# Optimization experiments

Measured on AMD Instinct MI355X. Metric: run time of the kernel, lower is better.

Reference implementation:

```python
import jax, jax.numpy as jnp
from jax import lax
import numpy as np

B, N, FIN, T, K, C_CHEB, F_TIME, STRIDE = 32, 900, 16, 24, 3, 64, 64, 1
LN_EPS = 1e-5


def _cheb_polys(L_tilde, K):
    # Faithful to repo: recurrence uses ELEMENTWISE multiply (np.ndarray '*').
    polys = [np.identity(N), np.asarray(L_tilde)]
    for i in range(2, K):
        polys.append(2 * L_tilde * polys[i - 1] - polys[i - 2])
    return np.stack(polys, axis=0).astype(np.float32)  # (K, N, N)


def setup_inputs() -> dict:
    key = jax.random.key(0)
    ks = jax.random.split(key, 6)
    rng = np.random.RandomState(0)
    A = rng.randn(N, N).astype(np.float32)
    L_tilde = (A + A.T) / (2.0 * np.sqrt(N))  # symmetric, entries O(1/sqrt(N))
    cheb = jnp.asarray(_cheb_polys(L_tilde, K))  # (K, N, N)
    x = jax.random.normal(ks[0], (B, N, FIN, T), dtype=jnp.float32)
    theta = jax.random.normal(ks[1], (K, FIN, C_CHEB), dtype=jnp.float32) * 0.1
    time_w = jax.random.normal(ks[2], (F_TIME, C_CHEB, 1, 3), dtype=jnp.float32) * 0.05
    time_b = jax.random.normal(ks[3], (F_TIME,), dtype=jnp.float32) * 0.01
    res_w = jax.random.normal(ks[4], (F_TIME, FIN, 1, 1), dtype=jnp.float32) * 0.1
    res_b = jax.random.normal(ks[5], (F_TIME,), dtype=jnp.float32) * 0.01
    gamma = jnp.ones((F_TIME,), dtype=jnp.float32)
    beta = jnp.zeros((F_TIME,), dtype=jnp.float32)
    return {"x": x, "cheb": cheb, "theta": theta, "time_w": time_w,
            "time_b": time_b, "res_w": res_w, "res_b": res_b,
            "gamma": gamma, "beta": beta}


def reference(x, cheb, theta, time_w, time_b, res_w, res_b, gamma, beta):
    b, n, f_in, t = x.shape
    # forward hardcodes spatial attention to ones
    spatial_at = jnp.ones((b, n, n), dtype=x.dtype)
    # Chebyshev graph conv with (trivial) spatial attention.
    # rhs[b,t,n,f] = sum_m (T_k * sA)[b,m,n] * x[b,m,f,t]
    out = jnp.zeros((b, t, n, theta.shape[-1]), dtype=x.dtype)
    for k in range(theta.shape[0]):
        Tk = cheb[k] * spatial_at                      # (B, N, N)
        rhs = jnp.einsum('bmn,bmft->btnf', Tk, x)      # (B, T, N, F_in)
        out = out + jnp.einsum('btnf,fc->btnc', rhs, theta[k])
    spatial_gcn = jax.nn.relu(out)                     # (B, T, N, C)
    # time conv over T axis: input layout (B, C, N, T), kernel (1,3), pad (0,1)
    g = jnp.transpose(spatial_gcn, (0, 3, 2, 1))       # (B, C, N, T)
    tc = lax.conv_general_dilated(g, time_w, window_strides=(1, STRIDE),
                                  padding=((0, 0), (1, 1)),
                                  dimension_numbers=('NCHW', 'OIHW', 'NCHW'))
    tc = tc + time_b[None, :, None, None]
    # residual 1x1 conv on raw input
    xr = jnp.transpose(x, (0, 2, 1, 3))                # (B, F_in, N, T)
    rc = lax.conv_general_dilated(xr, res_w, window_strides=(1, STRIDE),
                                  padding=((0, 0), (0, 0)),
                                  dimension_numbers=('NCHW', 'OIHW', 'NCHW'))
    rc = rc + res_b[None, :, None, None]
    y = jax.nn.relu(rc + tc)                           # (B, F_time, N, T)
    y = jnp.transpose(y, (0, 3, 2, 1))                 # (B, T, N, F_time)
    mu = jnp.mean(y, axis=-1, keepdims=True)
    var = jnp.mean(jnp.square(y - mu), axis=-1, keepdims=True)
    y_ln = (y - mu) * lax.rsqrt(var + LN_EPS) * gamma + beta
    return jnp.transpose(y_ln, (0, 2, 3, 1))           # (B, N, F_time, T)
```

## Files before the change

### kernel.cpp

```cpp
#include <hip/hip_runtime.h>
#include <hip/hip_bf16.h>

#define B_ 32
#define N_ 900
#define BN 8
#define NTILES 113
#define MS 16
#define MP 960

typedef __attribute__((ext_vector_type(8))) short bf16x8;
typedef __attribute__((ext_vector_type(16))) float f32x16;

#define OFF_XT 0u
#define OFF_CT 23592960u
#define OFF_XC 27279360u
#define OFF_TH 74465280u
#define OFF_TW 74472448u
#define WS_NEED 74500096u

__global__ __launch_bounds__(256)
void k0a_xT(const float* __restrict__ x, __hip_bfloat16* __restrict__ xT)
{
    __shared__ __hip_bfloat16 L[32][390];
    const int tid = threadIdx.x;
    const int m0 = blockIdx.x * 32, b = blockIdx.y;
#pragma unroll
    for (int it = 0; it < 12; ++it) {
        const int idx = tid + it * 256;
        const int mm = idx / 96, c4 = idx - mm * 96;
        float4 v = make_float4(0.f, 0.f, 0.f, 0.f);
        if (m0 + mm < N_)
            v = ((const float4*)(x + ((size_t)b * N_ + m0 + mm) * 384))[c4];
        L[mm][c4 * 4 + 0] = __float2bfloat16(v.x);
        L[mm][c4 * 4 + 1] = __float2bfloat16(v.y);
        L[mm][c4 * 4 + 2] = __float2bfloat16(v.z);
        L[mm][c4 * 4 + 3] = __float2bfloat16(v.w);
    }
    __syncthreads();
#pragma unroll
    for (int it = 0; it < 48; ++it) {
        const int idx = tid + it * 256;
        const int c = idx >> 5, mm = idx & 31;
        xT[((size_t)b * 384 + c) * MP + m0 + mm] = L[mm][c];
    }
}

__global__ __launch_bounds__(256)
void k0b_chebT(const float* __restrict__ cheb, __hip_bfloat16* __restrict__ chebT)
{
    __shared__ float L[32][33];
    const int tid = threadIdx.x;
    const int m0 = blockIdx.x * 32, n0 = blockIdx.y * 32, k = blockIdx.z;
#pragma unroll
    for (int it = 0; it < 4; ++it) {
        const int idx = tid + it * 256;
        const int mm = idx >> 5, nn = idx & 31;
        float v = 0.f;
        if (m0 + mm < N_ && n0 + nn < N_)
            v = cheb[(size_t)(k + 1) * (N_ * N_) + (size_t)(m0 + mm) * N_ + n0 + nn];
        L[mm][nn] = v;
    }
    __syncthreads();
#pragma unroll
    for (int it = 0; it < 4; ++it) {
        const int idx = tid + it * 256;
        const int nn = idx >> 5, mm = idx & 31;
        chebT[((size_t)k * MP + n0 + nn) * MP + m0 + mm] = __float2bfloat16(L[mm][nn]);
    }
}

__global__ __launch_bounds__(256)
void k0c_w(const float* __restrict__ tw, const float* __restrict__ rw,
           const float* __restrict__ th,
           __hip_bfloat16* __restrict__ thT, __hip_bfloat16* __restrict__ twB)
{
    const int tid = threadIdx.x;
    for (int i = tid; i < 64 * 56; i += 256) {
        const int c = i / 56, k = i - (i / 56) * 56;
        const float v = (k < 48) ? th[k * 64 + c] : 0.f;
        thT[i] = __float2bfloat16(v);
    }
    for (int i = tid; i < 64 * 216; i += 256) {
        const int co = i / 216, k = i - co * 216;
        float v = 0.f;
        if (k < 192)      v = tw[co * 192 + (k & 63) * 3 + (k >> 6)];
        else if (k < 208) v = rw[co * 16 + (k - 192)];
        twB[i] = __float2bfloat16(v);
    }
}

__global__ __launch_bounds__(256, 4)
void k1_mfma(const __hip_bfloat16* __restrict__ xT,
             const __hip_bfloat16* __restrict__ chebT,
             __hip_bfloat16* __restrict__ xcb)
{
    __shared__ __align__(16) __hip_bfloat16 At[2][64][72];
    __shared__ __align__(16) __hip_bfloat16 Bt[2][64][72];
    const int tid = threadIdx.x;
    const int id  = blockIdx.x;
    const int swz = (id & 7) * 720 + (id >> 3);
    const int n0 = (swz % 15) * 64;
    const int c0 = ((swz / 15) % 6) * 64;
    const int z  = swz / 90;
    const int b = z >> 1, k = z & 1;

    const int wid = tid >> 6, lane = tid & 63;
    const int wr = wid >> 1, wc = wid & 1;
    const int lr = lane & 31, hi = lane >> 5;

    const __hip_bfloat16* Asrc = chebT + ((size_t)k * MP + n0) * MP;
    const __hip_bfloat16* Bsrc = xT + ((size_t)b * 384 + c0) * MP;

    const int sr = tid >> 3, sc = (tid & 7) * 8;

    f32x16 acc;
#pragma unroll
    for (int j = 0; j < 16; ++j) acc[j] = 0.f;

    auto stage = [&](int buf, int m0) {
        *(int4*)&At[buf][sr][sc]      = *(const int4*)(Asrc + (size_t)sr * MP + m0 + sc);
        *(int4*)&At[buf][32 + sr][sc] = *(const int4*)(Asrc + (size_t)(32 + sr) * MP + m0 + sc);
        *(int4*)&Bt[buf][sr][sc]      = *(const int4*)(Bsrc + (size_t)sr * MP + m0 + sc);
        *(int4*)&Bt[buf][32 + sr][sc] = *(const int4*)(Bsrc + (size_t)(32 + sr) * MP + m0 + sc);
    };

    stage(0, 0);
    __syncthreads();
    const int ar = wr * 32 + lr, br = wc * 32 + lr;
    for (int s = 0; s < 15; ++s) {
        if (s + 1 < 15) stage((s + 1) & 1, (s + 1) * 64);
        const int cur = s & 1;
#pragma unroll
        for (int kk = 0; kk < 4; ++kk) {
            bf16x8 a  = *(const bf16x8*)&At[cur][ar][kk * 16 + hi * 8];
            bf16x8 bb = *(const bf16x8*)&Bt[cur][br][kk * 16 + hi * 8];
            acc = __builtin_amdgcn_mfma_f32_32x32x16_bf16(a, bb, acc, 0, 0, 0);
        }
        __syncthreads();
    }

    const int c = c0 + wc * 32 + lr;
    __hip_bfloat16* ob = xcb + ((size_t)(k * B_ + b)) * (MP * 384) + c;
#pragma unroll
    for (int reg = 0; reg < 16; ++reg) {
        const int row = n0 + wr * 32 + (reg & 3) + 8 * (reg >> 2) + 4 * hi;
        ob[(size_t)row * 384] = __float2bfloat16(acc[reg]);
    }
}

__global__ __launch_bounds__(384, 2)
void k2_mfma(const float* __restrict__ x,
             const __hip_bfloat16* __restrict__ xcb,
             const __hip_bfloat16* __restrict__ thT,
             const __hip_bfloat16* __restrict__ twB,
             const float* __restrict__ tb, const float* __restrict__ rb,
             const float* __restrict__ gam, const float* __restrict__ bet,
             float* __restrict__ out)
{
    __shared__ __align__(16) short xcL[2][8][384];
    __shared__ __align__(16) __hip_bfloat16 xbL[8][24][24];
    __shared__ __align__(16) __hip_bfloat16 gcnL[8][26][72];
    __shared__ __align__(16) __hip_bfloat16 twL[64][216];
    __shared__ float biasL[64], gamL[64], betL[64];

    const int tid = threadIdx.x;
    const int wid = tid >> 6, lane = tid & 63;
    const int l31 = lane & 31, hi = lane >> 5;
    const int n_base = blockIdx.x * BN;
    const int b = blockIdx.y;

    if (tid < 64) {
        biasL[tid] = tb[tid] + rb[tid];
        gamL[tid]  = gam[tid];
        betL[tid]  = bet[tid];
    }
    for (int i = tid; i < 1728; i += 384) ((int4*)twL)[i] = ((const int4*)twB)[i];
    for (int q = tid; q < 768; q += 384) {
        const int kk = q / 384, r = q - kk * 384;
        const int nl = r / 48, ch = r - nl * 48;
        ((int4*)xcL)[q] =
            *(const int4*)(xcb + (((size_t)(kk * B_ + b)) * MP + n_base + nl) * 384 + ch * 8);
    }
    for (int i = tid; i < 768; i += 384) {
        const int nl = i / 96, rem = i - nl * 96, f = rem / 6, t4 = rem - f * 6;
        const int ng = n_base + nl;
        float4 v = make_float4(0.f, 0.f, 0.f, 0.f);
        if (ng < N_)
            v = ((const float4*)(x + ((size_t)b * N_ + ng) * 384 + f * 24))[t4];
        xbL[nl][t4 * 4 + 0][f] = __float2bfloat16(v.x);
        xbL[nl][t4 * 4 + 1][f] = __float2bfloat16(v.y);
        xbL[nl][t4 * 4 + 2][f] = __float2bfloat16(v.z);
        xbL[nl][t4 * 4 + 3][f] = __float2bfloat16(v.w);
    }
    for (int i = tid; i < 1024; i += 384) {
        const int nl = i >> 7, c = (i >> 1) & 63, e = i & 1;
        gcnL[nl][e ? 25 : 0][c] = __float2bfloat16(0.f);
    }

    const int colA = wid * 32 + l31;
    const int nlA = colA / 24, tA = colA - nlA * 24;

    __syncthreads();

    const bf16x8 b0 = *(const bf16x8*)&xbL[nlA][tA][hi * 8];
    bf16x8 b1, b2;
#pragma unroll
    for (int j = 0; j < 8; ++j) {
        b1[j] = xcL[0][nlA][(hi * 8 + j) * 24 + tA];
        b2[j] = xcL[1][nlA][(hi * 8 + j) * 24 + tA];
    }

    {
        const short* thg = (const short*)thT;
        f32x16 a0, a1;
#pragma unroll
        for (int j = 0; j < 16; ++j) { a0[j] = 0.f; a1[j] = 0.f; }
        bf16x8 af;
        af = *(const bf16x8*)(thg + l31 * 56 + hi * 8);
        a0 = __builtin_amdgcn_mfma_f32_32x32x16_bf16(af, b0, a0, 0, 0, 0);
        af = *(const bf16x8*)(thg + l31 * 56 + 16 + hi * 8);
        a0 = __builtin_amdgcn_mfma_f32_32x32x16_bf16(af, b1, a0, 0, 0, 0);
        af = *(const bf16x8*)(thg + l31 * 56 + 32 + hi * 8);
        a0 = __builtin_amdgcn_mfma_f32_32x32x16_bf16(af, b2, a0, 0, 0, 0);
        af = *(const bf16x8*)(thg + (32 + l31) * 56 + hi * 8);
        a1 = __builtin_amdgcn_mfma_f32_32x32x16_bf16(af, b0, a1, 0, 0, 0);
        af = *(const bf16x8*)(thg + (32 + l31) * 56 + 16 + hi * 8);
        a1 = __builtin_amdgcn_mfma_f32_32x32x16_bf16(af, b1, a1, 0, 0, 0);
        af = *(const bf16x8*)(thg + (32 + l31) * 56 + 32 + hi * 8);
        a1 = __builtin_amdgcn_mfma_f32_32x32x16_bf16(af, b2, a1, 0, 0, 0);
#pragma unroll
        for (int reg = 0; reg < 16; ++reg) {
            const int cr = (reg & 3) + 8 * (reg >> 2) + 4 * hi;
            gcnL[nlA][tA + 1][cr]      = __float2bfloat16(fmaxf(a0[reg], 0.f));
            gcnL[nlA][tA + 1][32 + cr] = __float2bfloat16(fmaxf(a1[reg], 0.f));
        }
    }
    __syncthreads();

    f32x16 acc0, acc1;
#pragma unroll
    for (int j = 0; j < 16; ++j) { acc0[j] = 0.f; acc1[j] = 0.f; }
#pragma unroll
    for (int s = 0; s < 12; ++s) {
        const int dt  = s >> 2;
        const int ci0 = (s & 3) * 16 + hi * 8;
        const bf16x8 bb = *(const bf16x8*)&gcnL[nlA][tA + dt][ci0];
        const bf16x8 a0 = *(const bf16x8*)&twL[l31][dt * 64 + ci0];
        const bf16x8 a1 = *(const bf16x8*)&twL[32 + l31][dt * 64 + ci0];
        acc0 = __builtin_amdgcn_mfma_f32_32x32x16_bf16(a0, bb, acc0, 0, 0, 0);
        acc1 = __builtin_amdgcn_mfma_f32_32x32x16_bf16(a1, bb, acc1, 0, 0, 0);
    }
    {
        const bf16x8 a0 = *(const bf16x8*)&twL[l31][192 + hi * 8];
        const bf16x8 a1 = *(const bf16x8*)&twL[32 + l31][192 + hi * 8];
        acc0 = __builtin_amdgcn_mfma_f32_32x32x16_bf16(a0, b0, acc0, 0, 0, 0);
        acc1 = __builtin_amdgcn_mfma_f32_32x32x16_bf16(a1, b0, acc1, 0, 0, 0);
    }

    float y0[16], y1[16];
    float s1 = 0.f, s2 = 0.f;
#pragma unroll
    for (int reg = 0; reg < 16; ++reg) {
        const int cr = (reg & 3) + 8 * (reg >> 2) + 4 * hi;
        const float v0 = fmaxf(acc0[reg] + biasL[cr], 0.f);
        const float v1 = fmaxf(acc1[reg] + biasL[32 + cr], 0.f);
        y0[reg] = v0; y1[reg] = v1;
        s1 += v0 + v1;
        s2 += v0 * v0 + v1 * v1;
    }
    s1 += __shfl_xor(s1, 32);
    s2 += __shfl_xor(s2, 32);
    const float mu  = s1 * (1.f / 64.f);
    const float var = fmaxf(s2 * (1.f / 64.f) - mu * mu, 0.f);
    const float rs  = rsqrtf(var + 1e-5f);

    const int ng = n_base + nlA;
    if (ng < N_) {
        float* op = out + ((size_t)b * N_ + ng) * 1536 + tA;
#pragma unroll
        for (int reg = 0; reg < 16; ++reg) {
            const int cr = (reg & 3) + 8 * (reg >> 2) + 4 * hi;
            op[(size_t)cr * 24]        = (y0[reg] - mu) * rs * gamL[cr] + betL[cr];
            op[(size_t)(32 + cr) * 24] = (y1[reg] - mu) * rs * gamL[32 + cr] + betL[32 + cr];
        }
    }
}

__global__ __launch_bounds__(256, 2)
void astgcn_fused(const float* __restrict__ x, const float* __restrict__ cheb,
                  const float* __restrict__ theta, const float* __restrict__ tw,
                  const float* __restrict__ tb, const float* __restrict__ rw,
                  const float* __restrict__ rb, const float* __restrict__ gam,
                  const float* __restrict__ bet, float* __restrict__ out)
{
    __shared__ __align__(16) unsigned char smem[57152];
    float* xc   = (float*)smem;
    unsigned char* Y = smem + 24576;
    float* rwl  = (float*)(smem + 52032);
    float* misc = (float*)(smem + 56128);

    const int tid = threadIdx.x;
    const int n_base = blockIdx.x * BN;
    const int b = blockIdx.y;

    if (tid < 64) {
        misc[tid]       = tb[tid];
        misc[64 + tid]  = rb[tid];
        misc[128 + tid] = gam[tid];
        misc[192 + tid] = bet[tid];
    }
    for (int i = tid; i < 1024; i += 256) {
        const int co = i & 63, f = i >> 6;
        rwl[f * 64 + co] = rw[co * 16 + f];
    }

    float* xs  = (float*)Y;
    float* wls = (float*)(Y + 24576);
    const int nloc = tid >> 5;
    const int cg   = tid & 31;
    float a1[12], a2[12];
#pragma unroll
    for (int j = 0; j < 12; ++j) { a1[j] = 0.f; a2[j] = 0.f; }
    const float* xb = x + (size_t)b * N_ * 384;

    for (int mc = 0; mc < N_; mc += MS) {
        const int mlim = (N_ - mc) < MS ? (N_ - mc) : MS;
        __syncthreads();
        for (int i = tid; i < mlim * 96; i += 256) {
            const int mm = i / 96, c4 = i - mm * 96;
            ((float4*)(xs + mm * 384))[c4] =
                ((const float4*)(xb + (size_t)(mc + mm) * 384))[c4];
        }
        for (int i = tid; i < 2 * MS * 8; i += 256) {
            const int k = i >> 7, mm = (i >> 3) & 15, nn = i & 7;
            const int ng = n_base + nn;
            float wv = 0.f;
            if (mm < mlim && ng < N_)
                wv = cheb[(size_t)(k + 1) * (N_ * N_) + (size_t)(mc + mm) * N_ + ng];
            wls[(k * MS + mm) * 8 + nn] = wv;
        }
        __syncthreads();
        for (int mm = 0; mm < mlim; ++mm) {
            const float w1 = wls[mm * 8 + nloc];
            const float w2 = wls[(MS + mm) * 8 + nloc];
            const float* xr = xs + mm * 384 + (cg << 2);
#pragma unroll
            for (int seg = 0; seg < 3; ++seg) {
                const float4 v = *(const float4*)(xr + seg * 128);
                a1[seg*4+0] = fmaf(w1, v.x, a1[seg*4+0]);
                a1[seg*4+1] = fmaf(w1, v.y, a1[seg*4+1]);
                a1[seg*4+2] = fmaf(w1, v.z, a1[seg*4+2]);
                a1[seg*4+3] = fmaf(w1, v.w, a1[seg*4+3]);
                a2[seg*4+0] = fmaf(w2, v.x, a2[seg*4+0]);
                a2[seg*4+1] = fmaf(w2, v.y, a2[seg*4+1]);
                a2[seg*4+2] = fmaf(w2, v.z, a2[seg*4+2]);
                a2[seg*4+3] = fmaf(w2, v.w, a2[seg*4+3]);
            }
        }
    }
    __syncthreads();
#pragma unroll
    for (int seg = 0; seg < 3; ++seg) {
#pragma unroll
        for (int jj = 0; jj < 4; ++jj) {
            const int c = seg * 128 + (cg << 2) + jj;
            const int f = c / 24, t = c - f * 24;
            xc[(nloc * 24 + t) * 16 + f]        = a1[seg * 4 + jj];
            xc[((BN + nloc) * 24 + t) * 16 + f] = a2[seg * 4 + jj];
        }
    }
    __syncthreads();

    __hip_bfloat16* gcn = (__hip_bfloat16*)Y;
    {
        const int c2 = tid & 63;
        const int pg = tid >> 6;
        float th0r[16], th1r[16], th2r[16];
#pragma unroll
        for (int f = 0; f < 16; ++f) {
            th0r[f] = theta[f * 64 + c2];
            th1r[f] = theta[(16 + f) * 64 + c2];
            th2r[f] = theta[(32 + f) * 64 + c2];
        }
        for (int i = 0; i < 48; ++i) {
            const int p  = pg + 4 * i;
            const int nl = p / 24, t = p - nl * 24;
            const int ng = n_base + nl;
            float o = 0.f;
            if (ng < N_) {
                const float* xg = x + ((size_t)b * N_ + ng) * 384 + t;
                const float* x1 = xc + (nl * 24 + t) * 16;
                const float* x2 = xc + ((BN + nl) * 24 + t) * 16;
#pragma unroll
                for (int f = 0; f < 16; ++f)
                    o = fmaf(xg[f * 24], th0r[f], o);
#pragma unroll
                for (int f = 0; f < 16; ++f)
                    o = fmaf(x1[f], th1r[f], fmaf(x2[f], th2r[f], o));
            }
            o = fmaxf(o, 0.f);
            gcn[(nl * 26 + t + 1) * 66 + c2] = __float2bfloat16(o);
            if (t == 0)  gcn[(nl * 26) * 66 + c2]      = __float2bfloat16(0.f);
            if (t == 23) gcn[(nl * 26 + 25) * 66 + c2] = __float2bfloat16(0.f);
        }
    }

    const int nl3 = tid / 24, t3 = tid - nl3 * 24;
    const int ng3 = n_base + nl3;
    const bool act = (tid < 192) && (ng3 < N_);
    float acc[64];
#pragma unroll
    for (int co = 0; co < 64; ++co) acc[co] = misc[co] + misc[64 + co];
    if (act) {
        const float* xg = x + ((size_t)b * N_ + ng3) * 384 + t3;
#pragma unroll
        for (int f = 0; f < 16; ++f) {
            const float xv = xg[f * 24];
            const float* rp = rwl + f * 64;
#pragma unroll
            for (int co = 0; co < 64; ++co) acc[co] = fmaf(xv, rp[co], acc[co]);
        }
    }
    float* twl = xc;
#pragma unroll
    for (int half = 0; half < 2; ++half) {
        __syncthreads();
        for (int i = tid; i < 6144; i += 256)
            twl[i] = tw[((half * 32) + (i & 31)) * 192 + ((i >> 5) & 63) * 3 + (i >> 11)];
        __syncthreads();
        if (act) {
            const __hip_bfloat16* g0 = gcn + (nl3 * 26 + t3) * 66;
#pragma unroll
            for (int dt = 0; dt < 3; ++dt) {
                const __hip_bfloat16* grow = g0 + dt * 66;
                for (int ci = 0; ci < 64; ++ci) {
                    const float g = __bfloat162float(grow[ci]);
                    const float* twp = twl + (dt * 64 + ci) * 32;
#pragma unroll
                    for (int j = 0; j < 32; ++j)
                        acc[half * 32 + j] = fmaf(g, twp[j], acc[half * 32 + j]);
                }
            }
        }
    }
    if (act) {
        float mu = 0.f;
#pragma unroll
        for (int co = 0; co < 64; ++co) { acc[co] = fmaxf(acc[co], 0.f); mu += acc[co]; }
        mu *= (1.f / 64.f);
        float var = 0.f;
#pragma unroll
        for (int co = 0; co < 64; ++co) { const float d = acc[co] - mu; var = fmaf(d, d, var); }
        var *= (1.f / 64.f);
        const float rs = rsqrtf(var + 1e-5f);
        float* op = out + ((size_t)b * N_ + ng3) * (64 * 24) + t3;
#pragma unroll
        for (int co = 0; co < 64; ++co) {
            const float yl = (acc[co] - mu) * rs * misc[128 + co] + misc[192 + co];
            op[(size_t)co * 24] = yl;
        }
    }
}

extern "C" void kernel_launch(void* const* d_in, const int* in_sizes, int n_in,
                              void* d_out, int out_size, void* d_ws, size_t ws_size,
                              hipStream_t stream) {
    (void)out_size;
    const float *px = nullptr, *pcheb = nullptr, *pth = nullptr,
                *ptw = nullptr, *prw = nullptr;
    const float* p64[4] = {nullptr, nullptr, nullptr, nullptr};
    int n64 = 0;
    for (int i = 0; i < n_in; ++i) {
        const float* p = (const float*)d_in[i];
        switch (in_sizes[i]) {
            case 11059200: px    = p; break;
            case 2430000:  pcheb = p; break;
            case 3072:     pth   = p; break;
            case 12288:    ptw   = p; break;
            case 1024:     prw   = p; break;
            case 64:       if (n64 < 4) p64[n64] = p; ++n64; break;
            default: break;
        }
    }
    if (!px || !pcheb || !pth || !ptw || !prw || n64 != 4) {
        px    = (const float*)d_in[0]; pcheb = (const float*)d_in[1];
        pth   = (const float*)d_in[2]; ptw   = (const float*)d_in[3];
        p64[0] = (const float*)d_in[4]; prw  = (const float*)d_in[5];
        p64[1] = (const float*)d_in[6]; p64[2] = (const float*)d_in[7];
        p64[3] = (const float*)d_in[8];
    }
    float* out = (float*)d_out;

    if (ws_size >= (size_t)WS_NEED) {
        unsigned char* ws = (unsigned char*)d_ws;
        __hip_bfloat16* xT    = (__hip_bfloat16*)(ws + OFF_XT);
        __hip_bfloat16* chebT = (__hip_bfloat16*)(ws + OFF_CT);
        __hip_bfloat16* xcb   = (__hip_bfloat16*)(ws + OFF_XC);
        __hip_bfloat16* thT   = (__hip_bfloat16*)(ws + OFF_TH);
        __hip_bfloat16* twB   = (__hip_bfloat16*)(ws + OFF_TW);

        k0a_xT   <<<dim3(30, B_),     256, 0, stream>>>(px, xT);
        k0b_chebT<<<dim3(30, 30, 2),  256, 0, stream>>>(pcheb, chebT);
        k0c_w    <<<1,                256, 0, stream>>>(ptw, prw, pth, thT, twB);
        k1_mfma  <<<5760,             256, 0, stream>>>(xT, chebT, xcb);
        k2_mfma  <<<dim3(NTILES, B_), 384, 0, stream>>>(px, xcb, thT, twB,
                                                        p64[0], p64[1], p64[2], p64[3], out);
    } else {
        astgcn_fused<<<dim3(NTILES, B_), 256, 0, stream>>>(px, pcheb, pth, ptw,
                                                           p64[0], prw, p64[1],
                                                           p64[2], p64[3], out);
    }
}
```

Before: 219.2 us.

## Alias LDS regions in k2 to raise occupancy and stage coalesced output

Replaces the separate shared arrays in k2_mfma with one aliased LDS buffer. The time-conv weights are loaded in two phases into space reused from the xc/xb staging area, which reduces LDS footprint so launch bounds can ask for 5 blocks per CU instead of 2. The LayerNorm output is first written to LDS and then stored to global memory with 16-byte coalesced stores, replacing the strided scalar stores. The cost is several extra barriers, a split weight reload, and unaligned 8-byte LDS reads for the padded weight rows.

```diff
diff --git a/kernel.cpp b/kernel.cpp
--- a/kernel.cpp
+++ b/kernel.cpp
@@ -17,6 +17,15 @@
 #define OFF_TH 74465280u
 #define OFF_TW 74472448u
 #define WS_NEED 74500096u
+
+static __device__ __forceinline__ bf16x8 ld8_u8(const short* p) {
+    const short4 a = *(const short4*)p;
+    const short4 b = *(const short4*)(p + 4);
+    bf16x8 r;
+    r[0] = a.x; r[1] = a.y; r[2] = a.z; r[3] = a.w;
+    r[4] = b.x; r[5] = b.y; r[6] = b.z; r[7] = b.w;
+    return r;
+}
 
 __global__ __launch_bounds__(256)
 void k0a_xT(const float* __restrict__ x, __hip_bfloat16* __restrict__ xT)
@@ -148,7 +157,7 @@
     }
 }
 
-__global__ __launch_bounds__(384, 2)
+__global__ __launch_bounds__(384, 5)
 void k2_mfma(const float* __restrict__ x,
              const __hip_bfloat16* __restrict__ xcb,
              const __hip_bfloat16* __restrict__ thT,
@@ -157,11 +166,13 @@
              const float* __restrict__ gam, const float* __restrict__ bet,
              float* __restrict__ out)
 {
-    __shared__ __align__(16) short xcL[2][8][384];
-    __shared__ __align__(16) __hip_bfloat16 xbL[8][24][24];
-    __shared__ __align__(16) __hip_bfloat16 gcnL[8][26][72];
-    __shared__ __align__(16) __hip_bfloat16 twL[64][216];
-    __shared__ float biasL[64], gamL[64], betL[64];
+    __shared__ __align__(16) unsigned char smem[52224];
+    short* xcL           = (short*)smem;
+    __hip_bfloat16* xbL  = (__hip_bfloat16*)(smem + 12288);
+    short* twP           = (short*)smem;
+    __hip_bfloat16* gcnL = (__hip_bfloat16*)(smem + 21504);
+    float* misc          = (float*)(smem + 51456);
+    float* yF            = (float*)smem;
 
     const int tid = threadIdx.x;
     const int wid = tid >> 6, lane = tid & 63;
@@ -170,11 +181,10 @@
     const int b = blockIdx.y;
 
     if (tid < 64) {
-        biasL[tid] = tb[tid] + rb[tid];
-        gamL[tid]  = gam[tid];
-        betL[tid]  = bet[tid];
-    }
-    for (int i = tid; i < 1728; i += 384) ((int4*)twL)[i] = ((const int4*)twB)[i];
+        misc[tid]       = tb[tid] + rb[tid];
+        misc[64 + tid]  = gam[tid];
+        misc[128 + tid] = bet[tid];
+    }
     for (int q = tid; q < 768; q += 384) {
         const int kk = q / 384, r = q - kk * 384;
         const int nl = r / 48, ch = r - nl * 48;
@@ -187,14 +197,14 @@
         float4 v = make_float4(0.f, 0.f, 0.f, 0.f);
         if (ng < N_)
             v = ((const float4*)(x + ((size_t)b * N_ + ng) * 384 + f * 24))[t4];
-        xbL[nl][t4 * 4 + 0][f] = __float2bfloat16(v.x);
-        xbL[nl][t4 * 4 + 1][f] = __float2bfloat16(v.y);
-        xbL[nl][t4 * 4 + 2][f] = __float2bfloat16(v.z);
-        xbL[nl][t4 * 4 + 3][f] = __float2bfloat16(v.w);
+        xbL[nl * 576 + (t4 * 4 + 0) * 24 + f] = __float2bfloat16(v.x);
+        xbL[nl * 576 + (t4 * 4 + 1) * 24 + f] = __float2bfloat16(v.y);
+        xbL[nl * 576 + (t4 * 4 + 2) * 24 + f] = __float2bfloat16(v.z);
+        xbL[nl * 576 + (t4 * 4 + 3) * 24 + f] = __float2bfloat16(v.w);
     }
     for (int i = tid; i < 1024; i += 384) {
         const int nl = i >> 7, c = (i >> 1) & 63, e = i & 1;
-        gcnL[nl][e ? 25 : 0][c] = __float2bfloat16(0.f);
+        gcnL[(nl * 26 + (e ? 25 : 0)) * 72 + c] = __float2bfloat16(0.f);
     }
 
     const int colA = wid * 32 + l31;
@@ -202,12 +212,20 @@
 
     __syncthreads();
 
-    const bf16x8 b0 = *(const bf16x8*)&xbL[nlA][tA][hi * 8];
+    const bf16x8 b0 = *(const bf16x8*)&xbL[nlA * 576 + tA * 24 + hi * 8];
     bf16x8 b1, b2;
 #pragma unroll
     for (int j = 0; j < 8; ++j) {
-        b1[j] = xcL[0][nlA][(hi * 8 + j) * 24 + tA];
-        b2[j] = xcL[1][nlA][(hi * 8 + j) * 24 + tA];
+        b1[j] = xcL[nlA * 384 + (hi * 8 + j) * 24 + tA];
+        b2[j] = xcL[3072 + nlA * 384 + (hi * 8 + j) * 24 + tA];
+    }
+
+    __syncthreads();
+
+    for (int q = tid; q < 2048; q += 384) {
+        const int co = q >> 5, j = q & 31;
+        *(short4*)(twP + co * 140 + j * 4) =
+            *(const short4*)((const short*)twB + co * 216 + j * 4);
     }
 
     {
@@ -231,8 +249,8 @@
 #pragma unroll
         for (int reg = 0; reg < 16; ++reg) {
             const int cr = (reg & 3) + 8 * (reg >> 2) + 4 * hi;
-            gcnL[nlA][tA + 1][cr]      = __float2bfloat16(fmaxf(a0[reg], 0.f));
-            gcnL[nlA][tA + 1][32 + cr] = __float2bfloat16(fmaxf(a1[reg], 0.f));
+            gcnL[(nlA * 26 + tA + 1) * 72 + cr]      = __float2bfloat16(fmaxf(a0[reg], 0.f));
+            gcnL[(nlA * 26 + tA + 1) * 72 + 32 + cr] = __float2bfloat16(fmaxf(a1[reg], 0.f));
         }
     }
     __syncthreads();
@@ -241,30 +259,47 @@
 #pragma unroll
     for (int j = 0; j < 16; ++j) { acc0[j] = 0.f; acc1[j] = 0.f; }
 #pragma unroll
-    for (int s = 0; s < 12; ++s) {
+    for (int s = 0; s < 8; ++s) {
         const int dt  = s >> 2;
         const int ci0 = (s & 3) * 16 + hi * 8;
-        const bf16x8 bb = *(const bf16x8*)&gcnL[nlA][tA + dt][ci0];
-        const bf16x8 a0 = *(const bf16x8*)&twL[l31][dt * 64 + ci0];
-        const bf16x8 a1 = *(const bf16x8*)&twL[32 + l31][dt * 64 + ci0];
+        const bf16x8 bb = *(const bf16x8*)&gcnL[(nlA * 26 + tA + dt) * 72 + ci0];
+        const bf16x8 a0 = ld8_u8(twP + l31 * 140 + dt * 64 + ci0);
+        const bf16x8 a1 = ld8_u8(twP + (32 + l31) * 140 + dt * 64 + ci0);
         acc0 = __builtin_amdgcn_mfma_f32_32x32x16_bf16(a0, bb, acc0, 0, 0, 0);
         acc1 = __builtin_amdgcn_mfma_f32_32x32x16_bf16(a1, bb, acc1, 0, 0, 0);
     }
+    __syncthreads();
+
+    for (int q = tid; q < 1280; q += 384) {
+        const int co = q / 20, j = q - co * 20;
+        *(short4*)(twP + co * 140 + j * 4) =
+            *(const short4*)((const short*)twB + co * 216 + 128 + j * 4);
+    }
+    __syncthreads();
+
+#pragma unroll
+    for (int s = 0; s < 4; ++s) {
+        const int ci0 = s * 16 + hi * 8;
+        const bf16x8 bb = *(const bf16x8*)&gcnL[(nlA * 26 + tA + 2) * 72 + ci0];
+        const bf16x8 a0 = ld8_u8(twP + l31 * 140 + ci0);
+        const bf16x8 a1 = ld8_u8(twP + (32 + l31) * 140 + ci0);
+        acc0 = __builtin_amdgcn_mfma_f32_32x32x16_bf16(a0, bb, acc0, 0, 0, 0);
+        acc1 = __builtin_amdgcn_mfma_f32_32x32x16_bf16(a1, bb, acc1, 0, 0, 0);
+    }
     {
-        const bf16x8 a0 = *(const bf16x8*)&twL[l31][192 + hi * 8];
-        const bf16x8 a1 = *(const bf16x8*)&twL[32 + l31][192 + hi * 8];
+        const bf16x8 a0 = ld8_u8(twP + l31 * 140 + 64 + hi * 8);
+        const bf16x8 a1 = ld8_u8(twP + (32 + l31) * 140 + 64 + hi * 8);
         acc0 = __builtin_amdgcn_mfma_f32_32x32x16_bf16(a0, b0, acc0, 0, 0, 0);
         acc1 = __builtin_amdgcn_mfma_f32_32x32x16_bf16(a1, b0, acc1, 0, 0, 0);
     }
 
-    float y0[16], y1[16];
     float s1 = 0.f, s2 = 0.f;
 #pragma unroll
     for (int reg = 0; reg < 16; ++reg) {
         const int cr = (reg & 3) + 8 * (reg >> 2) + 4 * hi;
-        const float v0 = fmaxf(acc0[reg] + biasL[cr], 0.f);
-        const float v1 = fmaxf(acc1[reg] + biasL[32 + cr], 0.f);
-        y0[reg] = v0; y1[reg] = v1;
+        const float v0 = fmaxf(acc0[reg] + misc[cr], 0.f);
+        const float v1 = fmaxf(acc1[reg] + misc[32 + cr], 0.f);
+        acc0[reg] = v0; acc1[reg] = v1;
         s1 += v0 + v1;
         s2 += v0 * v0 + v1 * v1;
     }
@@ -274,15 +309,22 @@
     const float var = fmaxf(s2 * (1.f / 64.f) - mu * mu, 0.f);
     const float rs  = rsqrtf(var + 1e-5f);
 
-    const int ng = n_base + nlA;
-    if (ng < N_) {
-        float* op = out + ((size_t)b * N_ + ng) * 1536 + tA;
-#pragma unroll
-        for (int reg = 0; reg < 16; ++reg) {
-            const int cr = (reg & 3) + 8 * (reg >> 2) + 4 * hi;
-            op[(size_t)cr * 24]        = (y0[reg] - mu) * rs * gamL[cr] + betL[cr];
-            op[(size_t)(32 + cr) * 24] = (y1[reg] - mu) * rs * gamL[32 + cr] + betL[32 + cr];
-        }
+    __syncthreads();
+#pragma unroll
+    for (int reg = 0; reg < 16; ++reg) {
+        const int cr = (reg & 3) + 8 * (reg >> 2) + 4 * hi;
+        yF[nlA * 1536 + cr * 24 + tA] =
+            (acc0[reg] - mu) * rs * misc[64 + cr] + misc[128 + cr];
+        yF[nlA * 1536 + (32 + cr) * 24 + tA] =
+            (acc1[reg] - mu) * rs * misc[64 + 32 + cr] + misc[128 + 32 + cr];
+    }
+    __syncthreads();
+
+    float* ob = out + ((size_t)b * N_ + n_base) * 1536;
+    for (int i = tid; i < 3072; i += 384) {
+        const int nl = i / 384;
+        if (n_base + nl < N_)
+            ((int4*)ob)[i] = ((const int4*)yF)[i];
     }
 }
 
```

Result: slower. 260.4 us (+18.8%).

## Enlarge k1 MFMA tile to 192x128 with 512 threads and 3 accumulators per wave

Applied to the files above, without the earlier changes.

Restructures the Chebyshev graph-conv GEMM kernel from 64x64 tiles with 256 threads to 192x128 tiles with 512 threads. Each wave now holds three 32x32 accumulators and reuses one B fragment across them, and the K step drops from 64 to 32. The grid shrinks from 5760 to 960 blocks and the swizzle is adjusted to match. The aim is to cut global and LDS traffic per MFMA through higher operand reuse. In exchange it uses more registers, fewer blocks for load balancing across CUs, and twice as many sync iterations.

```diff
diff --git a/kernel.cpp b/kernel.cpp
--- a/kernel.cpp
+++ b/kernel.cpp
@@ -89,52 +89,63 @@
     }
 }
 
-__global__ __launch_bounds__(256, 4)
+__global__ __launch_bounds__(512)
 void k1_mfma(const __hip_bfloat16* __restrict__ xT,
              const __hip_bfloat16* __restrict__ chebT,
              __hip_bfloat16* __restrict__ xcb)
 {
-    __shared__ __align__(16) __hip_bfloat16 At[2][64][72];
-    __shared__ __align__(16) __hip_bfloat16 Bt[2][64][72];
+    __shared__ __align__(16) __hip_bfloat16 At[2][192][40];
+    __shared__ __align__(16) __hip_bfloat16 Bt[2][128][40];
     const int tid = threadIdx.x;
     const int id  = blockIdx.x;
-    const int swz = (id & 7) * 720 + (id >> 3);
-    const int n0 = (swz % 15) * 64;
-    const int c0 = ((swz / 15) % 6) * 64;
-    const int z  = swz / 90;
+    const int swz  = (id & 7) * 120 + (id >> 3);
+    const int tile = swz % 15;
+    const int z    = swz / 15;
+    const int n0 = (tile % 5) * 192;
+    const int c0 = (tile / 5) * 128;
     const int b = z >> 1, k = z & 1;
 
     const int wid = tid >> 6, lane = tid & 63;
-    const int wr = wid >> 1, wc = wid & 1;
+    const int wr = wid & 1, wc = wid >> 1;
     const int lr = lane & 31, hi = lane >> 5;
 
     const __hip_bfloat16* Asrc = chebT + ((size_t)k * MP + n0) * MP;
     const __hip_bfloat16* Bsrc = xT + ((size_t)b * 384 + c0) * MP;
 
-    const int sr = tid >> 3, sc = (tid & 7) * 8;
-
-    f32x16 acc;
-#pragma unroll
-    for (int j = 0; j < 16; ++j) acc[j] = 0.f;
+    f32x16 acc[3];
+#pragma unroll
+    for (int rb = 0; rb < 3; ++rb)
+#pragma unroll
+        for (int j = 0; j < 16; ++j) acc[rb][j] = 0.f;
 
     auto stage = [&](int buf, int m0) {
-        *(int4*)&At[buf][sr][sc]      = *(const int4*)(Asrc + (size_t)sr * MP + m0 + sc);
-        *(int4*)&At[buf][32 + sr][sc] = *(const int4*)(Asrc + (size_t)(32 + sr) * MP + m0 + sc);
-        *(int4*)&Bt[buf][sr][sc]      = *(const int4*)(Bsrc + (size_t)sr * MP + m0 + sc);
-        *(int4*)&Bt[buf][32 + sr][sc] = *(const int4*)(Bsrc + (size_t)(32 + sr) * MP + m0 + sc);
+        for (int q = tid; q < 768; q += 512) {
+            const int r = q >> 2, c8 = (q & 3) * 8;
+            *(int4*)&At[buf][r][c8] = *(const int4*)(Asrc + (size_t)r * MP + m0 + c8);
+        }
+        {
+            const int q = tid;
+            if (q < 512) {
+                const int r = q >> 2, c8 = (q & 3) * 8;
+                *(int4*)&Bt[buf][r][c8] = *(const int4*)(Bsrc + (size_t)r * MP + m0 + c8);
+            }
+        }
     };
 
     stage(0, 0);
     __syncthreads();
-    const int ar = wr * 32 + lr, br = wc * 32 + lr;
-    for (int s = 0; s < 15; ++s) {
-        if (s + 1 < 15) stage((s + 1) & 1, (s + 1) * 64);
+    for (int s = 0; s < 30; ++s) {
+        if (s + 1 < 30) stage((s + 1) & 1, (s + 1) * 32);
         const int cur = s & 1;
 #pragma unroll
-        for (int kk = 0; kk < 4; ++kk) {
-            bf16x8 a  = *(const bf16x8*)&At[cur][ar][kk * 16 + hi * 8];
-            bf16x8 bb = *(const bf16x8*)&Bt[cur][br][kk * 16 + hi * 8];
-            acc = __builtin_amdgcn_mfma_f32_32x32x16_bf16(a, bb, acc, 0, 0, 0);
+        for (int ks = 0; ks < 2; ++ks) {
+            const bf16x8 bb = *(const bf16x8*)&Bt[cur][wc * 32 + lr][ks * 16 + hi * 8];
+#pragma unroll
+            for (int rb = 0; rb < 3; ++rb) {
+                const bf16x8 a =
+                    *(const bf16x8*)&At[cur][wr * 96 + rb * 32 + lr][ks * 16 + hi * 8];
+                acc[rb] = __builtin_amdgcn_mfma_f32_32x32x16_bf16(a, bb, acc[rb], 0, 0, 0);
+            }
         }
         __syncthreads();
     }
@@ -142,10 +153,12 @@
     const int c = c0 + wc * 32 + lr;
     __hip_bfloat16* ob = xcb + ((size_t)(k * B_ + b)) * (MP * 384) + c;
 #pragma unroll
-    for (int reg = 0; reg < 16; ++reg) {
-        const int row = n0 + wr * 32 + (reg & 3) + 8 * (reg >> 2) + 4 * hi;
-        ob[(size_t)row * 384] = __float2bfloat16(acc[reg]);
-    }
+    for (int rb = 0; rb < 3; ++rb)
+#pragma unroll
+        for (int reg = 0; reg < 16; ++reg) {
+            const int row = n0 + wr * 96 + rb * 32 + (reg & 3) + 8 * (reg >> 2) + 4 * hi;
+            ob[(size_t)row * 384] = __float2bfloat16(acc[rb][reg]);
+        }
 }
 
 __global__ __launch_bounds__(384, 2)
@@ -502,7 +515,7 @@
         k0a_xT   <<<dim3(30, B_),     256, 0, stream>>>(px, xT);
         k0b_chebT<<<dim3(30, 30, 2),  256, 0, stream>>>(pcheb, chebT);
         k0c_w    <<<1,                256, 0, stream>>>(ptw, prw, pth, thT, twB);
-        k1_mfma  <<<5760,             256, 0, stream>>>(xT, chebT, xcb);
+        k1_mfma  <<<960,              512, 0, stream>>>(xT, chebT, xcb);
         k2_mfma  <<<dim3(NTILES, B_), 384, 0, stream>>>(px, xcb, thT, twB,
                                                         p64[0], p64[1], p64[2], p64[3], out);
     } else {
```

Result: faster. 212.4 us (-3.1%).
